# Kernel tuning notes

Hardware: AMD Instinct MI355X
Metric: run time of the kernel (lower is better)

## Reference

```python
import jax, jax.numpy as jnp
import numpy as np

# pars (match init_kwargs)
ALPHA, BETA = 0.9, 0.8            # synaptic / membrane decay (snn.Synaptic)
THRESHOLD = 1.0
BETA_PLUS, BETA_MINUS = 0.9, 0.9  # pre / post trace decay
A_PLUS, A_MINUS = 0.008, 0.0066   # STDP learning rates
W_MIN, W_MAX = 0.0, 1.0
NUM_STEPS, INPUT_SIZE, N_NEURONS = 256, 784, 512
SPIKE_RATE = 0.1                  # Bernoulli rate for the input spike train


def setup_inputs() -> dict:
    key = jax.random.key(0)
    k1, k2 = jax.random.split(key)
    # binary pre-synaptic spike train [num_steps, input_size]
    image = (jax.random.uniform(k1, (NUM_STEPS, INPUT_SIZE)) < SPIKE_RATE).astype(jnp.float32)
    # fc.weight, clamped into [w_min, w_max] as in __init__
    W = jax.random.uniform(k2, (N_NEURONS, INPUT_SIZE), minval=W_MIN, maxval=W_MAX)
    return {"image": image, "W": W}


def reference(image, W):
    """Faithful scan over time of: Linear -> Synaptic LIF (subtract reset) ->
    post-trace update -> classic STDP weight update with clamp.
    Returns (W_rec, spk_rec, mem_rec, syn_rec, post_rec) stacked over time."""
    dtype = image.dtype
    n = W.shape[0]
    d = image.shape[1]
    syn0 = jnp.zeros((n,), dtype)
    mem0 = jnp.zeros((n,), dtype)
    spk0 = jnp.zeros((n,), dtype)   # previous spike -> reset term
    post0 = jnp.zeros((n,), dtype)  # post-synaptic trace
    pre0 = jnp.zeros((d,), dtype)   # pre-synaptic trace (generate_traces: trace[0]=0)

    def step(carry, x_t):
        syn, mem, spk_prev, post, pre_tr, Wc = carry
        # fc (no bias)
        I = Wc @ x_t                                   # [n_neurons]
        # snntorch Synaptic, reset_mechanism='subtract' (reset from prev-step mem)
        syn = ALPHA * syn + I
        mem = BETA * mem + syn - spk_prev * THRESHOLD
        spk = (mem > THRESHOLD).astype(dtype)
        # post-synaptic trace update (before STDP, as in forward)
        post = BETA_MINUS * post + spk
        # classic STDP
        ltp = A_PLUS * jnp.outer(spk, pre_tr)          # [n, d]
        ltd = A_MINUS * jnp.outer(post, x_t)           # [n, d]
        Wn = jnp.clip(Wc + ltp - ltd, W_MIN, W_MAX)
        # pre-trace recurrence: trace[t+1] = beta_plus*trace[t] + image[t]
        pre_new = BETA_PLUS * pre_tr + x_t
        return (syn, mem, spk, post, pre_new, Wn), (spk, mem, syn, post, Wn)

    _, (spk_rec, mem_rec, syn_rec, post_rec, W_rec) = jax.lax.scan(
        step, (syn0, mem0, spk0, post0, pre0, W), image)
    return W_rec, spk_rec, mem_rec, syn_rec, post_rec
```

## Files before the change

kernel.cpp:

```cpp
#include <hip/hip_runtime.h>
#include <hip/hip_bf16.h>
#include <stdint.h>

#define NUM_STEPS  256
#define INPUT_SIZE 784
#define N_NEURONS  512
#define CHUNKS     196

__device__ __forceinline__ float bf2f(unsigned short u) {
    union { uint32_t i; float f; } v; v.i = ((uint32_t)u) << 16; return v.f;
}
__device__ __forceinline__ unsigned short f2bf(float f) {
    union { float f; uint32_t i; } v; v.f = f;
    uint32_t x = v.i;
    uint32_t r = (x + 0x7fffu + ((x >> 16) & 1u)) >> 16;
    return (unsigned short)r;
}

template <bool F32>
__device__ void scan_run(const void* __restrict__ img_v,
                         const void* __restrict__ W_v,
                         void* __restrict__ out_v)
{
    const int row  = blockIdx.x;
    const int tid  = threadIdx.x;
    const bool act = tid < CHUNKS;
    const int col4 = tid << 2;
    const int wave = tid >> 6;
    const int lane = tid & 63;

    __shared__ float red[2][4];

    const size_t WREC = (size_t)NUM_STEPS * N_NEURONS * INPUT_SIZE;
    const size_t SREC = (size_t)NUM_STEPS * N_NEURONS;

    float w0 = 0.f, w1 = 0.f, w2 = 0.f, w3 = 0.f;
    float p0 = 0.f, p1 = 0.f, p2 = 0.f, p3 = 0.f;
    if (act) {
        if constexpr (F32) {
            const float* W0 = (const float*)W_v;
            const float4 wv = *(const float4*)(W0 + (size_t)row * INPUT_SIZE + col4);
            w0 = wv.x; w1 = wv.y; w2 = wv.z; w3 = wv.w;
        } else {
            const unsigned short* W0 = (const unsigned short*)W_v;
            const ushort4 wv = *(const ushort4*)(W0 + (size_t)row * INPUT_SIZE + col4);
            w0 = bf2f(wv.x); w1 = bf2f(wv.y); w2 = bf2f(wv.z); w3 = bf2f(wv.w);
        }
    }

    float syn = 0.f, mem = 0.f, spk_prev = 0.f, post = 0.f;

    for (int t = 0; t < NUM_STEPS; ++t) {
        float x0 = 0.f, x1 = 0.f, x2 = 0.f, x3 = 0.f;
        float partial = 0.f;
        if (act) {
            if constexpr (F32) {
                const float* img = (const float*)img_v;
                const float4 xv = *(const float4*)(img + (size_t)t * INPUT_SIZE + col4);
                x0 = xv.x; x1 = xv.y; x2 = xv.z; x3 = xv.w;
            } else {
                const unsigned short* img = (const unsigned short*)img_v;
                const ushort4 xv = *(const ushort4*)(img + (size_t)t * INPUT_SIZE + col4);
                x0 = bf2f(xv.x); x1 = bf2f(xv.y); x2 = bf2f(xv.z); x3 = bf2f(xv.w);
            }
            partial = w0 * x0 + w1 * x1 + w2 * x2 + w3 * x3;
        }
        #pragma unroll
        for (int off = 32; off > 0; off >>= 1)
            partial += __shfl_down(partial, off, 64);
        if (lane == 0) red[t & 1][wave] = partial;
        __syncthreads();
        const float I = red[t & 1][0] + red[t & 1][1] + red[t & 1][2] + red[t & 1][3];

        syn = 0.9f * syn + I;
        mem = 0.8f * mem + syn - spk_prev;
        const float spk = (mem > 1.0f) ? 1.0f : 0.0f;
        post = 0.9f * post + spk;
        const float ap = 0.008f  * spk;
        const float am = 0.0066f * post;

        const size_t r = (size_t)t * N_NEURONS + row;
        if (act) {
            w0 = fminf(fmaxf(w0 + ap * p0 - am * x0, 0.f), 1.f);
            w1 = fminf(fmaxf(w1 + ap * p1 - am * x1, 0.f), 1.f);
            w2 = fminf(fmaxf(w2 + ap * p2 - am * x2, 0.f), 1.f);
            w3 = fminf(fmaxf(w3 + ap * p3 - am * x3, 0.f), 1.f);

            if constexpr (F32) {
                float* out = (float*)out_v;
                *(float4*)(out + r * INPUT_SIZE + col4) = make_float4(w0, w1, w2, w3);
            } else {
                unsigned short* out = (unsigned short*)out_v;
                ushort4 ov;
                ov.x = f2bf(w0); ov.y = f2bf(w1); ov.z = f2bf(w2); ov.w = f2bf(w3);
                *(ushort4*)(out + r * INPUT_SIZE + col4) = ov;
            }

            p0 = 0.9f * p0 + x0;
            p1 = 0.9f * p1 + x1;
            p2 = 0.9f * p2 + x2;
            p3 = 0.9f * p3 + x3;
        }
        if (tid == 0) {
            if constexpr (F32) {
                float* out = (float*)out_v;
                out[WREC + 0 * SREC + r] = spk;
                out[WREC + 1 * SREC + r] = mem;
                out[WREC + 2 * SREC + r] = syn;
                out[WREC + 3 * SREC + r] = post;
            } else {
                unsigned short* out = (unsigned short*)out_v;
                out[WREC + 0 * SREC + r] = f2bf(spk);
                out[WREC + 1 * SREC + r] = f2bf(mem);
                out[WREC + 2 * SREC + r] = f2bf(syn);
                out[WREC + 3 * SREC + r] = f2bf(post);
            }
        }
        spk_prev = spk;
    }
}

__global__ __launch_bounds__(256) void snn_row_scan_kernel(
    const void* __restrict__ img,
    const void* __restrict__ W,
    void* __restrict__ out)
{
    const unsigned short* w16 = (const unsigned short*)W;
    bool f32 = false;
    for (int i = 0; i < 128; ++i) f32 |= (w16[i] > 0x3F80u);
    if (f32) scan_run<true >(img, W, out);
    else     scan_run<false>(img, W, out);
}

extern "C" void kernel_launch(void* const* d_in, const int* in_sizes, int n_in,
                              void* d_out, int out_size, void* d_ws, size_t ws_size,
                              hipStream_t stream) {
    (void)in_sizes; (void)n_in; (void)d_ws; (void)ws_size; (void)out_size;
    snn_row_scan_kernel<<<dim3(N_NEURONS), dim3(256), 0, stream>>>(d_in[0], d_in[1], d_out);
}
```

Measured before the change: 667.0 us.

## Use one wavefront per neuron row with shuffle reduction and image prefetch

Each neuron row is now handled by a single 64-lane wavefront holding four 4-wide chunks per lane, instead of a 256-thread block. The per-step dot product is reduced with xor shuffles alone, which removes the shared-memory reduction and the block-wide barrier. The next time step's image chunk is loaded before the current step's math so its latency overlaps with compute. The trade-off is fewer threads per block (512 single-wave blocks) and more registers per lane, which may reduce the in-flight stores available to saturate the large W_rec write bandwidth.

New measurement: 649.4 us. 1.03x faster.

```diff
diff --git a/kernel.cpp b/kernel.cpp
--- a/kernel.cpp
+++ b/kernel.cpp
@@ -1,11 +1,9 @@
 #include <hip/hip_runtime.h>
-#include <hip/hip_bf16.h>
 #include <stdint.h>
 
 #define NUM_STEPS  256
 #define INPUT_SIZE 784
 #define N_NEURONS  512
-#define CHUNKS     196
 
 __device__ __forceinline__ float bf2f(unsigned short u) {
     union { uint32_t i; float f; } v; v.i = ((uint32_t)u) << 16; return v.f;
@@ -13,8 +11,29 @@
 __device__ __forceinline__ unsigned short f2bf(float f) {
     union { float f; uint32_t i; } v; v.f = f;
     uint32_t x = v.i;
-    uint32_t r = (x + 0x7fffu + ((x >> 16) & 1u)) >> 16;
-    return (unsigned short)r;
+    return (unsigned short)((x + 0x7fffu + ((x >> 16) & 1u)) >> 16);
+}
+
+template <bool F32>
+__device__ __forceinline__ void ld_chunk(const void* __restrict__ base, size_t elem, float* d) {
+    if constexpr (F32) {
+        const float4 v = *(const float4*)((const float*)base + elem);
+        d[0] = v.x; d[1] = v.y; d[2] = v.z; d[3] = v.w;
+    } else {
+        const ushort4 v = *(const ushort4*)((const unsigned short*)base + elem);
+        d[0] = bf2f(v.x); d[1] = bf2f(v.y); d[2] = bf2f(v.z); d[3] = bf2f(v.w);
+    }
+}
+
+template <bool F32>
+__device__ __forceinline__ void st_chunk(void* __restrict__ base, size_t elem, const float* s) {
+    if constexpr (F32) {
+        *(float4*)((float*)base + elem) = make_float4(s[0], s[1], s[2], s[3]);
+    } else {
+        ushort4 v;
+        v.x = f2bf(s[0]); v.y = f2bf(s[1]); v.z = f2bf(s[2]); v.w = f2bf(s[3]);
+        *(ushort4*)((unsigned short*)base + elem) = v;
+    }
 }
 
 template <bool F32>
@@ -23,54 +42,54 @@
                          void* __restrict__ out_v)
 {
     const int row  = blockIdx.x;
-    const int tid  = threadIdx.x;
-    const bool act = tid < CHUNKS;
-    const int col4 = tid << 2;
-    const int wave = tid >> 6;
-    const int lane = tid & 63;
-
-    __shared__ float red[2][4];
+    const int lane = threadIdx.x;
+    const bool has4 = lane < 4;
 
     const size_t WREC = (size_t)NUM_STEPS * N_NEURONS * INPUT_SIZE;
     const size_t SREC = (size_t)NUM_STEPS * N_NEURONS;
 
-    float w0 = 0.f, w1 = 0.f, w2 = 0.f, w3 = 0.f;
-    float p0 = 0.f, p1 = 0.f, p2 = 0.f, p3 = 0.f;
-    if (act) {
-        if constexpr (F32) {
-            const float* W0 = (const float*)W_v;
-            const float4 wv = *(const float4*)(W0 + (size_t)row * INPUT_SIZE + col4);
-            w0 = wv.x; w1 = wv.y; w2 = wv.z; w3 = wv.w;
-        } else {
-            const unsigned short* W0 = (const unsigned short*)W_v;
-            const ushort4 wv = *(const ushort4*)(W0 + (size_t)row * INPUT_SIZE + col4);
-            w0 = bf2f(wv.x); w1 = bf2f(wv.y); w2 = bf2f(wv.z); w3 = bf2f(wv.w);
-        }
+    size_t cofs[4];
+    cofs[0] = (size_t)(lane      ) * 4;
+    cofs[1] = (size_t)(lane +  64) * 4;
+    cofs[2] = (size_t)(lane + 128) * 4;
+    cofs[3] = (size_t)(192 + lane) * 4;
+
+    float w[4][4], p[4][4], x[4][4], xn[4][4];
+    #pragma unroll
+    for (int c = 0; c < 4; ++c)
+        #pragma unroll
+        for (int j = 0; j < 4; ++j) { w[c][j] = 0.f; p[c][j] = 0.f; x[c][j] = 0.f; xn[c][j] = 0.f; }
+
+    {
+        const size_t wbase = (size_t)row * INPUT_SIZE;
+        #pragma unroll
+        for (int c = 0; c < 3; ++c) ld_chunk<F32>(W_v, wbase + cofs[c], w[c]);
+        if (has4) ld_chunk<F32>(W_v, wbase + cofs[3], w[3]);
+        #pragma unroll
+        for (int c = 0; c < 3; ++c) ld_chunk<F32>(img_v, cofs[c], x[c]);
+        if (has4) ld_chunk<F32>(img_v, cofs[3], x[3]);
     }
 
     float syn = 0.f, mem = 0.f, spk_prev = 0.f, post = 0.f;
 
     for (int t = 0; t < NUM_STEPS; ++t) {
-        float x0 = 0.f, x1 = 0.f, x2 = 0.f, x3 = 0.f;
+        if (t + 1 < NUM_STEPS) {
+            const size_t xbase = (size_t)(t + 1) * INPUT_SIZE;
+            #pragma unroll
+            for (int c = 0; c < 3; ++c) ld_chunk<F32>(img_v, xbase + cofs[c], xn[c]);
+            if (has4) ld_chunk<F32>(img_v, xbase + cofs[3], xn[3]);
+        }
+
         float partial = 0.f;
-        if (act) {
-            if constexpr (F32) {
-                const float* img = (const float*)img_v;
-                const float4 xv = *(const float4*)(img + (size_t)t * INPUT_SIZE + col4);
-                x0 = xv.x; x1 = xv.y; x2 = xv.z; x3 = xv.w;
-            } else {
-                const unsigned short* img = (const unsigned short*)img_v;
-                const ushort4 xv = *(const ushort4*)(img + (size_t)t * INPUT_SIZE + col4);
-                x0 = bf2f(xv.x); x1 = bf2f(xv.y); x2 = bf2f(xv.z); x3 = bf2f(xv.w);
-            }
-            partial = w0 * x0 + w1 * x1 + w2 * x2 + w3 * x3;
-        }
         #pragma unroll
-        for (int off = 32; off > 0; off >>= 1)
-            partial += __shfl_down(partial, off, 64);
-        if (lane == 0) red[t & 1][wave] = partial;
-        __syncthreads();
-        const float I = red[t & 1][0] + red[t & 1][1] + red[t & 1][2] + red[t & 1][3];
+        for (int c = 0; c < 4; ++c)
+            #pragma unroll
+            for (int j = 0; j < 4; ++j) partial += w[c][j] * x[c][j];
+
+        #pragma unroll
+        for (int off = 1; off < 64; off <<= 1)
+            partial += __shfl_xor(partial, off, 64);
+        const float I = partial;
 
         syn = 0.9f * syn + I;
         mem = 0.8f * mem + syn - spk_prev;
@@ -79,29 +98,20 @@
         const float ap = 0.008f  * spk;
         const float am = 0.0066f * post;
 
-        const size_t r = (size_t)t * N_NEURONS + row;
-        if (act) {
-            w0 = fminf(fmaxf(w0 + ap * p0 - am * x0, 0.f), 1.f);
-            w1 = fminf(fmaxf(w1 + ap * p1 - am * x1, 0.f), 1.f);
-            w2 = fminf(fmaxf(w2 + ap * p2 - am * x2, 0.f), 1.f);
-            w3 = fminf(fmaxf(w3 + ap * p3 - am * x3, 0.f), 1.f);
+        const size_t r     = (size_t)t * N_NEURONS + row;
+        const size_t obase = r * INPUT_SIZE;
 
-            if constexpr (F32) {
-                float* out = (float*)out_v;
-                *(float4*)(out + r * INPUT_SIZE + col4) = make_float4(w0, w1, w2, w3);
-            } else {
-                unsigned short* out = (unsigned short*)out_v;
-                ushort4 ov;
-                ov.x = f2bf(w0); ov.y = f2bf(w1); ov.z = f2bf(w2); ov.w = f2bf(w3);
-                *(ushort4*)(out + r * INPUT_SIZE + col4) = ov;
-            }
+        #pragma unroll
+        for (int c = 0; c < 4; ++c)
+            #pragma unroll
+            for (int j = 0; j < 4; ++j)
+                w[c][j] = fminf(fmaxf(w[c][j] + ap * p[c][j] - am * x[c][j], 0.f), 1.f);
 
-            p0 = 0.9f * p0 + x0;
-            p1 = 0.9f * p1 + x1;
-            p2 = 0.9f * p2 + x2;
-            p3 = 0.9f * p3 + x3;
-        }
-        if (tid == 0) {
+        #pragma unroll
+        for (int c = 0; c < 3; ++c) st_chunk<F32>(out_v, obase + cofs[c], w[c]);
+        if (has4) st_chunk<F32>(out_v, obase + cofs[3], w[3]);
+
+        if (lane == 0) {
             if constexpr (F32) {
                 float* out = (float*)out_v;
                 out[WREC + 0 * SREC + r] = spk;
@@ -116,11 +126,19 @@
                 out[WREC + 3 * SREC + r] = f2bf(post);
             }
         }
+
+        #pragma unroll
+        for (int c = 0; c < 4; ++c)
+            #pragma unroll
+            for (int j = 0; j < 4; ++j) {
+                p[c][j] = 0.9f * p[c][j] + x[c][j];
+                x[c][j] = xn[c][j];
+            }
         spk_prev = spk;
     }
 }
 
-__global__ __launch_bounds__(256) void snn_row_scan_kernel(
+__global__ __launch_bounds__(64) void snn_row_scan_kernel(
     const void* __restrict__ img,
     const void* __restrict__ W,
     void* __restrict__ out)
@@ -136,5 +154,5 @@
                               void* d_out, int out_size, void* d_ws, size_t ws_size,
                               hipStream_t stream) {
     (void)in_sizes; (void)n_in; (void)d_ws; (void)ws_size; (void)out_size;
-    snn_row_scan_kernel<<<dim3(N_NEURONS), dim3(256), 0, stream>>>(d_in[0], d_in[1], d_out);
+    snn_row_scan_kernel<<<dim3(N_NEURONS), dim3(64), 0, stream>>>(d_in[0], d_in[1], d_out);
 }
```
